# Performance work log

Hardware: AMD Instinct MI355X
Metric: run time of the kernel (lower is better)

The kernel has to match this reference:

```python
import jax, jax.numpy as jnp
import numpy as np

KS, AS = 13, 12  # kernel_size (12 vertices + center), anchor_size (icosahedron vertices)


def _icosa():
    # Icosahedron oriented with vertex 0 on +z (required by sort_level_vs xy-rotation logic)
    r5 = np.sqrt(5.0); rr = 2.0 / r5
    vs = [[0.0, 0.0, 1.0]]
    for k in range(5):
        t = 2.0 * np.pi * k / 5.0
        vs.append([rr * np.cos(t), rr * np.sin(t), 1.0 / r5])
    for k in range(5):
        t = 2.0 * np.pi * k / 5.0 + np.pi / 5.0
        vs.append([rr * np.cos(t), rr * np.sin(t), -1.0 / r5])
    vs.append([0.0, 0.0, -1.0])
    return np.array(vs)


def _rotm(axis, ang):
    a = np.asarray(axis, dtype=np.float64); a = a / np.linalg.norm(a)
    K = np.array([[0, -a[2], a[1]], [a[2], 0, -a[0]], [-a[1], a[0], 0]])
    return np.eye(3) + np.sin(ang) * K + (1.0 - np.cos(ang)) * (K @ K)


def _ico_group(vs):
    # Generate the 60-element icosahedral rotation group by closure from two generators
    gens = [_rotm([0.0, 0.0, 1.0], 2 * np.pi / 5), _rotm(vs[1], 2 * np.pi / 5)]
    group = [np.eye(3)]
    keys = {tuple(np.round(np.eye(3), 4).ravel())}
    frontier = [np.eye(3)]
    while frontier:
        nxt = []
        for g in frontier:
            for h in gens:
                c = h @ g
                k = tuple(np.round(c, 4).ravel())
                if k not in keys:
                    keys.add(k); group.append(c); nxt.append(c)
        frontier = nxt
    return group


def _sort_level_vs(v_idxs, vs):
    # Faithful port of sort_level_vs: order ring vertices by successive 72-deg xy rotations
    out = [v_idxs[0]]
    vs_l = vs[v_idxs][:, :2]
    cur = vs_l[[0]]
    dth = 2 * np.pi / 5
    R = np.array([[np.cos(dth), -np.sin(dth)], [np.sin(dth), np.cos(dth)]])
    for _ in range(4):
        cur = R.dot(cur.T).T
        out.append(v_idxs[np.argmin(np.abs(vs_l - cur).sum(1))])
    return np.array(out)


def _build_buffers():
    vs = _icosa()
    dots = vs @ vs.T
    v0_adjs = np.where(np.abs(dots[0] - 1.0 / np.sqrt(5)) < 1e-6)[0]
    v0_lv2 = np.where(np.abs(dots[0] + 1.0 / np.sqrt(5)) < 1e-6)[0]
    v0_opp = int(np.argmin(dots[0]))
    # 12 rotation anchors: one group element mapping vertex 0 to each vertex
    group = _ico_group(vs)
    vRs = []
    for i in range(12):
        for R in group:
            if np.linalg.norm(R @ vs[0] - vs[i]) < 1e-5:
                vRs.append(R); break
    vRs = np.stack(vRs)  # [12,3,3]
    rot_v = np.einsum('rij,aj->rai', vRs, vs)  # [12,12,3]
    d = np.linalg.norm(rot_v[:, :, None, :] - vs[None, None], axis=-1)
    trace_idx_ori = np.argmin(d, axis=2)  # [12,12] vertex permutation per anchor rotation
    trace_idx_rot = np.empty_like(trace_idx_ori)
    for r in range(12):
        trace_idx_rot[r, trace_idx_ori[r]] = np.arange(12)
    trace_idxv_rot = np.concatenate([trace_idx_rot, np.full((12, 1), 12, np.int64)], axis=1)  # [12,13]
    # idx_map: faithful port of the __init__ construction (maps 13*12 slots -> 36 weight params)
    inv = np.empty(12, np.int64)
    inv[0] = 0; inv[v0_adjs] = 1; inv[v0_lv2] = 2; inv[v0_opp] = 3
    a_s = _sort_level_vs(v0_adjs, vs)
    l_s = _sort_level_vs(v0_lv2, vs)
    idx_map = np.empty(KS * AS, np.int64)
    idx_map[:AS] = inv
    idx_map[v0_opp * AS:(v0_opp + 1) * AS] = inv + 4
    idx_map[-AS:] = inv + 8
    seq1 = np.arange(12, 24); seq2 = np.arange(24, 36)
    idx_map[a_s[0] * AS:(a_s[0] + 1) * AS] = seq1
    idx_map[l_s[0] * AS:(l_s[0] + 1) * AS] = seq2
    shifts = [[4, 0, 1, 2, 3], [3, 4, 0, 1, 2], [2, 3, 4, 0, 1], [1, 2, 3, 4, 0]]
    for j, sh in enumerate(shifts, start=1):
        new = np.empty(12, np.int64)
        new[a_s] = a_s[sh]; new[l_s] = l_s[sh]
        new[0] = 0; new[v0_opp] = v0_opp
        idx_map[a_s[j] * AS:(a_s[j] + 1) * AS] = seq1[new]
        idx_map[l_s[j] * AS:(l_s[j] + 1) * AS] = seq2[new]
    return idx_map, trace_idxv_rot, trace_idx_rot


def setup_inputs() -> dict:
    key = jax.random.key(0)
    k1, k2 = jax.random.split(key)
    B, CIN, COUT, P = 8, 16, 16, 4096
    x = jax.random.normal(k1, (B, CIN, KS, P, AS), dtype=jnp.float32)
    W = jax.random.normal(k2, (COUT, CIN, 36), dtype=jnp.float32) * 0.05  # xavier-scale
    idx_map, tivr, tir = _build_buffers()
    return {
        'x': x,
        'W': W,
        'idx_map': jnp.asarray(idx_map, jnp.int32),
        'trace_idxv_rot': jnp.asarray(tivr, jnp.int32),
        'trace_idx_rot': jnp.asarray(tir, jnp.int32),
    }


def reference(x, W, idx_map, trace_idxv_rot, trace_idx_rot):
    d_out, d_in, _ = W.shape
    # Expand 36 free params to the [d, c, k, a] kernel via idx_map gather
    Wm = W[:, :, idx_map].reshape(d_out, d_in, KS, AS)
    # The two torch.gather calls (dims 2 then 3) collapse to:
    # Wfull[d,c,k,a,r] = Wm[d,c, trace_idxv_rot[r,k], trace_idx_rot[r,a]]
    Wfull = Wm[:, :, trace_idxv_rot[:, :, None], trace_idx_rot[:, None, :]]  # [d,c,r,k,a]
    return jnp.einsum('dcrka,bckpa->bdpr', Wfull, x)
```

## Files before the change

### kernel.cpp

```cpp
#include <hip/hip_runtime.h>
#include <stdint.h>

#define CIN_  16
#define KS_   13
#define AS_   12
#define R_    12
#define KT    96
#define NSTEP 26
#define LDP   104

typedef float  f32x4  __attribute__((ext_vector_type(4)));
typedef __bf16 bf16x4 __attribute__((ext_vector_type(4)));
typedef __bf16 bf16x8 __attribute__((ext_vector_type(8)));

__global__ void build_wmatf(const float* __restrict__ W,
                            const int* __restrict__ idx_map,
                            const int* __restrict__ tivr,
                            const int* __restrict__ tir,
                            __bf16* __restrict__ WmatF) {
  int gid  = blockIdx.x * blockDim.x + threadIdx.x;
  int lane = gid & 63;
  int fid  = gid >> 6;
  int kt   = fid / 36;
  int rem  = fid - kt * 36;
  int w    = rem / 9;
  int sub  = rem - w * 9;
  int mtl  = sub / 3;
  int ks   = sub - mtl * 3;
  int mt   = w * 3 + mtl;

  int row = mt * 16 + (lane & 15);
  int d = row / R_;
  int r = row - d * R_;

  bf16x8 v;
#pragma unroll
  for (int e = 0; e < 8; ++e) {
    int kap = kt * KT + ks * 32 + (lane >> 4) * 8 + e;
    int c = kap / (KS_ * AS_);
    int t = kap - c * (KS_ * AS_);
    int k = t / AS_;
    int a = t - k * AS_;
    int s = idx_map[tivr[r * KS_ + k] * AS_ + tir[r * AS_ + a]];
    v[e] = (__bf16)W[(d * CIN_ + c) * 36 + s];
  }
  *(bf16x8*)(WmatF + (size_t)gid * 8) = v;
}

__global__ __launch_bounds__(256, 2)
void s2conv(const float* __restrict__ x,
            const __bf16* __restrict__ WmatF,
            float* __restrict__ out) {
  __shared__ __bf16 Xs[2][64][LDP];

  const int tid  = threadIdx.x;
  const int lane = tid & 63;
  const int wave = tid >> 6;
  const int l15  = lane & 15;
  const int l4   = lane >> 4;

  const int wg = blockIdx.x;
  const int b  = wg >> 6;
  const int p0 = (wg & 63) << 6;

  f32x4 acc[3][4];
#pragma unroll
  for (int i = 0; i < 3; ++i)
#pragma unroll
    for (int j = 0; j < 4; ++j)
      acc[i][j] = f32x4{0.f, 0.f, 0.f, 0.f};

  const char* aBase = (const char*)WmatF + (size_t)wave * 9216 + lane * 16;
  auto loadA = [&](int kt, bf16x8 (&af)[9]) {
    const char* gk = aBase + (size_t)kt * 36864;
#pragma unroll
    for (int f = 0; f < 9; ++f)
      af[f] = *(const bf16x8*)(gk + f * 1024);
  };

  const char* xb = (const char*)x + ((size_t)b * 208) * 49152 * 4
                   + (size_t)p0 * 48;
  auto load_x = [&](int kt, f32x4 (&st)[6]) {
#pragma unroll
    for (int h = 0; h < 2; ++h) {
      const char* bp = xb + ((size_t)(kt * 8 + wave * 2 + h)) * (49152 * 4);
#pragma unroll
      for (int j = 0; j < 3; ++j)
        st[h * 3 + j] = *(const f32x4*)(bp + (j * 64 + lane) * 16);
    }
  };

  auto write_X = [&](int buf, f32x4 (&st)[6]) {
    char* xsb = (char*)&Xs[buf][0][0];
#pragma unroll
    for (int h = 0; h < 2; ++h) {
      int ck12 = (wave * 2 + h) * 12;
#pragma unroll
      for (int j = 0; j < 3; ++j) {
        int f4i = j * 64 + lane;
        int pl  = f4i / 3;
        int a   = (f4i - pl * 3) * 4;
        bf16x4 v = __builtin_convertvector(st[h * 3 + j], bf16x4);
        *(bf16x4*)(xsb + (pl * LDP + ck12 + a) * 2) = v;
      }
    }
  };

  auto mfma_phase = [&](int buf, bf16x8 (&af)[9]) {
    const __bf16* xsb = &Xs[buf][0][0];
#pragma unroll
    for (int ks = 0; ks < 3; ++ks) {
      bf16x8 bfr[4];
#pragma unroll
      for (int nt = 0; nt < 4; ++nt)
        bfr[nt] = *(const bf16x8*)(xsb + (nt * 16 + l15) * LDP
                                       + ks * 32 + l4 * 8);
#pragma unroll
      for (int mtl = 0; mtl < 3; ++mtl)
#pragma unroll
        for (int nt = 0; nt < 4; ++nt)
          acc[mtl][nt] = __builtin_amdgcn_mfma_f32_16x16x32_bf16(
              af[mtl * 3 + ks], bfr[nt], acc[mtl][nt], 0, 0, 0);
    }
  };

  auto barrier = [&]() {
    asm volatile("s_waitcnt lgkmcnt(0)" ::: "memory");
    __builtin_amdgcn_s_barrier();
  };

  f32x4  s0[6], s1[6];
  bf16x8 aE[9], aO[9];
  load_x(0, s0);
  load_x(1, s1);
  loadA(0, aE);
  __builtin_amdgcn_sched_barrier(0);
  write_X(0, s0);
  barrier();

#pragma unroll 1
  for (int t = 0; t < 24; t += 2) {
    load_x(t + 2, s0);
    loadA(t + 1, aO);
    __builtin_amdgcn_sched_barrier(0);
    write_X(1, s1);
    mfma_phase(0, aE);
    barrier();

    load_x(t + 3, s1);
    loadA(t + 2, aE);
    __builtin_amdgcn_sched_barrier(0);
    write_X(0, s0);
    mfma_phase(1, aO);
    barrier();
  }

  loadA(25, aO);
  __builtin_amdgcn_sched_barrier(0);
  write_X(1, s1);
  mfma_phase(0, aE);
  barrier();
  mfma_phase(1, aO);

#pragma unroll
  for (int mtl = 0; mtl < 3; ++mtl) {
    int mrow0 = wave * 48 + mtl * 16 + l4 * 4;
    int d  = mrow0 / 12;
    int r0 = mrow0 - d * 12;
#pragma unroll
    for (int nt = 0; nt < 4; ++nt) {
      int p = p0 + nt * 16 + l15;
      float* dst = out + (size_t)((b * 16 + d) * 4096 + p) * 12 + r0;
      *(f32x4*)dst = acc[mtl][nt];
    }
  }
}

extern "C" void kernel_launch(void* const* d_in, const int* in_sizes, int n_in,
                              void* d_out, int out_size, void* d_ws, size_t ws_size,
                              hipStream_t stream) {
  const float* x       = (const float*)d_in[0];
  const float* W       = (const float*)d_in[1];
  const int*   idx_map = (const int*)d_in[2];
  const int*   tivr    = (const int*)d_in[3];
  const int*   tir     = (const int*)d_in[4];
  float*       out     = (float*)d_out;
  __bf16*      WmatF   = (__bf16*)d_ws;

  build_wmatf<<<dim3(117), dim3(512), 0, stream>>>(W, idx_map, tivr, tir, WmatF);
  s2conv<<<dim3(512), dim3(256), 0, stream>>>(x, WmatF, out);
}
```

Before: 80.99 us.

## Halve pixel tile per block, single-buffer weight fragments, raise occupancy

Each block now handles 32 pixels instead of 64, so the grid doubles to 1024 blocks and launch bounds allow 4 blocks per CU. The weight fragments keep one register set and are reloaded right after each MFMA phase instead of being double-buffered. The x load mapping is recomputed for the smaller tile. The goal is more parallelism and occupancy to hide memory latency, at the cost of re-reading the weight matrix twice as often and exposing the A-load latency before the next phase.

```diff
diff --git a/kernel.cpp b/kernel.cpp
--- a/kernel.cpp
+++ b/kernel.cpp
@@ -47,11 +47,11 @@
   *(bf16x8*)(WmatF + (size_t)gid * 8) = v;
 }
 
-__global__ __launch_bounds__(256, 2)
+__global__ __launch_bounds__(256, 4)
 void s2conv(const float* __restrict__ x,
             const __bf16* __restrict__ WmatF,
             float* __restrict__ out) {
-  __shared__ __bf16 Xs[2][64][LDP];
+  __shared__ __bf16 Xs[2][32][LDP];
 
   const int tid  = threadIdx.x;
   const int lane = tid & 63;
@@ -60,67 +60,68 @@
   const int l4   = lane >> 4;
 
   const int wg = blockIdx.x;
-  const int b  = wg >> 6;
-  const int p0 = (wg & 63) << 6;
+  const int b  = wg >> 7;
+  const int p0 = (wg & 127) << 5;
 
-  f32x4 acc[3][4];
+  int xck[3], xr[3], xpl[3], xa[3];
+#pragma unroll
+  for (int j = 0; j < 3; ++j) {
+    int g = j * 256 + tid;
+    xck[j] = g / 96;
+    xr[j]  = g - xck[j] * 96;
+    xpl[j] = xr[j] / 3;
+    xa[j]  = (xr[j] - xpl[j] * 3) * 4;
+  }
+  const char* xb = (const char*)x +
+      ((size_t)b * 208 * 49152 + (size_t)p0 * 12) * 4;
+
+  f32x4 acc[3][2];
 #pragma unroll
   for (int i = 0; i < 3; ++i)
 #pragma unroll
-    for (int j = 0; j < 4; ++j)
+    for (int j = 0; j < 2; ++j)
       acc[i][j] = f32x4{0.f, 0.f, 0.f, 0.f};
 
   const char* aBase = (const char*)WmatF + (size_t)wave * 9216 + lane * 16;
-  auto loadA = [&](int kt, bf16x8 (&af)[9]) {
+  bf16x8 aA[9];
+  auto loadA = [&](int kt) {
     const char* gk = aBase + (size_t)kt * 36864;
 #pragma unroll
     for (int f = 0; f < 9; ++f)
-      af[f] = *(const bf16x8*)(gk + f * 1024);
+      aA[f] = *(const bf16x8*)(gk + f * 1024);
   };
 
-  const char* xb = (const char*)x + ((size_t)b * 208) * 49152 * 4
-                   + (size_t)p0 * 48;
-  auto load_x = [&](int kt, f32x4 (&st)[6]) {
+  auto load_x = [&](int kt, f32x4 (&st)[3]) {
 #pragma unroll
-    for (int h = 0; h < 2; ++h) {
-      const char* bp = xb + ((size_t)(kt * 8 + wave * 2 + h)) * (49152 * 4);
+    for (int j = 0; j < 3; ++j)
+      st[j] = *(const f32x4*)(xb + (size_t)(kt * 8 + xck[j]) * 196608
+                                  + xr[j] * 16);
+  };
+
+  auto write_X = [&](int buf, f32x4 (&st)[3]) {
+    char* xsb = (char*)&Xs[buf][0][0];
 #pragma unroll
-      for (int j = 0; j < 3; ++j)
-        st[h * 3 + j] = *(const f32x4*)(bp + (j * 64 + lane) * 16);
+    for (int j = 0; j < 3; ++j) {
+      bf16x4 v = __builtin_convertvector(st[j], bf16x4);
+      *(bf16x4*)(xsb + (xpl[j] * LDP + xck[j] * 12 + xa[j]) * 2) = v;
     }
   };
 
-  auto write_X = [&](int buf, f32x4 (&st)[6]) {
-    char* xsb = (char*)&Xs[buf][0][0];
-#pragma unroll
-    for (int h = 0; h < 2; ++h) {
-      int ck12 = (wave * 2 + h) * 12;
-#pragma unroll
-      for (int j = 0; j < 3; ++j) {
-        int f4i = j * 64 + lane;
-        int pl  = f4i / 3;
-        int a   = (f4i - pl * 3) * 4;
-        bf16x4 v = __builtin_convertvector(st[h * 3 + j], bf16x4);
-        *(bf16x4*)(xsb + (pl * LDP + ck12 + a) * 2) = v;
-      }
-    }
-  };
-
-  auto mfma_phase = [&](int buf, bf16x8 (&af)[9]) {
+  auto mfma_phase = [&](int buf) {
     const __bf16* xsb = &Xs[buf][0][0];
 #pragma unroll
     for (int ks = 0; ks < 3; ++ks) {
-      bf16x8 bfr[4];
+      bf16x8 bfr[2];
 #pragma unroll
-      for (int nt = 0; nt < 4; ++nt)
+      for (int nt = 0; nt < 2; ++nt)
         bfr[nt] = *(const bf16x8*)(xsb + (nt * 16 + l15) * LDP
                                        + ks * 32 + l4 * 8);
 #pragma unroll
       for (int mtl = 0; mtl < 3; ++mtl)
 #pragma unroll
-        for (int nt = 0; nt < 4; ++nt)
+        for (int nt = 0; nt < 2; ++nt)
           acc[mtl][nt] = __builtin_amdgcn_mfma_f32_16x16x32_bf16(
-              af[mtl * 3 + ks], bfr[nt], acc[mtl][nt], 0, 0, 0);
+              aA[mtl * 3 + ks], bfr[nt], acc[mtl][nt], 0, 0, 0);
     }
   };
 
@@ -129,11 +130,10 @@
     __builtin_amdgcn_s_barrier();
   };
 
-  f32x4  s0[6], s1[6];
-  bf16x8 aE[9], aO[9];
+  f32x4 s0[3], s1[3];
   load_x(0, s0);
+  loadA(0);
   load_x(1, s1);
-  loadA(0, aE);
   __builtin_amdgcn_sched_barrier(0);
   write_X(0, s0);
   barrier();
@@ -141,26 +141,25 @@
 #pragma unroll 1
   for (int t = 0; t < 24; t += 2) {
     load_x(t + 2, s0);
-    loadA(t + 1, aO);
     __builtin_amdgcn_sched_barrier(0);
     write_X(1, s1);
-    mfma_phase(0, aE);
+    mfma_phase(0);
+    loadA(t + 1);
     barrier();
 
     load_x(t + 3, s1);
-    loadA(t + 2, aE);
     __builtin_amdgcn_sched_barrier(0);
     write_X(0, s0);
-    mfma_phase(1, aO);
+    mfma_phase(1);
+    loadA(t + 2);
     barrier();
   }
 
-  loadA(25, aO);
-  __builtin_amdgcn_sched_barrier(0);
   write_X(1, s1);
-  mfma_phase(0, aE);
+  mfma_phase(0);
+  loadA(25);
   barrier();
-  mfma_phase(1, aO);
+  mfma_phase(1);
 
 #pragma unroll
   for (int mtl = 0; mtl < 3; ++mtl) {
@@ -168,7 +167,7 @@
     int d  = mrow0 / 12;
     int r0 = mrow0 - d * 12;
 #pragma unroll
-    for (int nt = 0; nt < 4; ++nt) {
+    for (int nt = 0; nt < 2; ++nt) {
       int p = p0 + nt * 16 + l15;
       float* dst = out + (size_t)((b * 16 + d) * 4096 + p) * 12 + r0;
       *(f32x4*)dst = acc[mtl][nt];
@@ -188,5 +187,5 @@
   __bf16*      WmatF   = (__bf16*)d_ws;
 
   build_wmatf<<<dim3(117), dim3(512), 0, stream>>>(W, idx_map, tivr, tir, WmatF);
-  s2conv<<<dim3(512), dim3(256), 0, stream>>>(x, WmatF, out);
+  s2conv<<<dim3(1024), dim3(256), 0, stream>>>(x, WmatF, out);
 }
```

Result: slower. 92.89 us (+14.7%).
